# Kernel optimization log

Hardware: AMD Instinct MI355X
Metric: run time of the kernel (lower is better)

The kernel has to match this reference:

```python
import jax, jax.numpy as jnp
from jax import lax
import numpy as np

N, T, D_IN = 2048, 256, 3
H, I, D_OUT = 256, 512, 5


def setup_inputs() -> dict:
    key = jax.random.key(0)
    ks = jax.random.split(key, 9)
    s_h = 1.0 / np.sqrt(H)
    s_i = 1.0 / np.sqrt(I)
    return {
        "x": jax.random.normal(ks[0], (N, T, D_IN), dtype=jnp.float32),
        # PyTorch LSTMCell params, gate order i,f,g,o stacked along dim 0
        "W_ih": jax.random.uniform(ks[1], (4 * H, D_IN), jnp.float32, -s_h, s_h),
        "W_hh": jax.random.uniform(ks[2], (4 * H, H), jnp.float32, -s_h, s_h),
        "b_ih": jax.random.uniform(ks[3], (4 * H,), jnp.float32, -s_h, s_h),
        "b_hh": jax.random.uniform(ks[4], (4 * H,), jnp.float32, -s_h, s_h),
        "W1": jax.random.uniform(ks[5], (I, H), jnp.float32, -s_h, s_h),
        "b1": jax.random.uniform(ks[6], (I,), jnp.float32, -s_h, s_h),
        "W2": jax.random.uniform(ks[7], (D_OUT, I), jnp.float32, -s_i, s_i),
        "b2": jax.random.uniform(ks[8], (D_OUT,), jnp.float32, -s_i, s_i),
    }


def reference(x, W_ih, W_hh, b_ih, b_hh, W1, b1, W2, b2):
    n, t, _ = x.shape
    h_dim = W_hh.shape[1]
    # Precompute input contribution to gates for all timesteps: [T, N, 4H]
    xg = jnp.einsum('ntd,gd->tng', x, W_ih) + (b_ih + b_hh)

    def step(carry, xt):
        h, c = carry
        gates = xt + h @ W_hh.T  # [N, 4H]
        i, f, g, o = jnp.split(gates, 4, axis=-1)
        i = jax.nn.sigmoid(i)
        f = jax.nn.sigmoid(f)
        g = jnp.tanh(g)
        o = jax.nn.sigmoid(o)
        c = f * c + i * g
        h = o * jnp.tanh(c)
        return (h, c), h

    h0 = jnp.zeros((n, h_dim), dtype=x.dtype)
    c0 = jnp.zeros((n, h_dim), dtype=x.dtype)
    (hs_final, cs_final), hs_stack = lax.scan(step, (h0, c0), xg)  # hs_stack [T,N,H]

    out = jax.nn.relu(hs_stack @ W1.T + b1) @ W2.T + b2  # [T, N, 5]
    return jnp.transpose(out, (1, 0, 2)), hs_final, cs_final
```

## Files before the change

### kernel.cpp

```cpp
#include <hip/hip_runtime.h>


typedef __attribute__((ext_vector_type(8))) short bf16x8;
typedef __attribute__((ext_vector_type(4))) float f32x4;
typedef __attribute__((ext_vector_type(4))) int   i32x4;
typedef unsigned long long ull;

#define HST 272
#define HBS 296
#define M1S 520
#define USHB 16384
#define HSOFF 2621440
#define CSOFF 3145728
#define I8S_OFF   0
#define I8P_OFF   131072
#define TRL_OFF   262144
#define W1_OFF    278528
#define WEIGHTS_B 573440ull
#define CSTATE_F  524288
#define STATE_B   4194304ull
#define H_OFF_B   (WEIGHTS_B + STATE_B)
#define SM_PIN 0
#define SM_TRL 131072
#define SM_HBI 139264
#define SM_HBL 147968
#define SM_XS  156672
#define SM_TOTAL 162816
#define SM_AS 0
#define SM_M1 37888
#define SM_W2 104448

__device__ __forceinline__ unsigned short f2bf(float f) {
    unsigned u = __builtin_bit_cast(unsigned, f);
    u += 0x7fffu + ((u >> 16) & 1u);
    return (unsigned short)(u >> 16);
}
__device__ __forceinline__ float bf2f(unsigned short s) {
    unsigned u = ((unsigned)s) << 16;
    return __builtin_bit_cast(float, u);
}
__device__ __forceinline__ float sigm(float v)  { return 1.0f / (1.0f + __expf(-v)); }
__device__ __forceinline__ float tanh_(float v) { return 1.0f - 2.0f / (1.0f + __expf(2.0f * v)); }
__device__ __forceinline__ f32x4 MF(bf16x8 a, bf16x8 b, f32x4 c) {
    return __builtin_amdgcn_mfma_f32_16x16x32_bf16(a, b, c, 0, 0, 0);
}
__device__ __forceinline__ i32x4 MFI(i32x4 a, i32x4 b, i32x4 c) {
    return __builtin_amdgcn_mfma_i32_16x16x64_i8(a, b, c, 0, 0, 0);
}

__global__ void __launch_bounds__(1024) prep_gates_i8(
    const float* __restrict__ Whh, char* __restrict__ ws8)
{
    const int u = (int)blockIdx.x;
    const int q = u >> 2, kt = u & 3;
    const int tid = (int)threadIdx.x;
    const int wv = tid >> 6, l = tid & 63;
    size_t base = (q < 2) ? (size_t)I8P_OFF : (size_t)I8S_OFF;
    base += (size_t)(q & 1) * 65536;
    const int col = q * 256 + wv * 16 + (l & 15);
    const int kb  = kt * 64 + (l >> 4) * 16;
    union { char c[16]; i32x4 v; } p;
#pragma unroll
    for (int e = 0; e < 16; ++e) {
        float w = Whh[col * 256 + kb + e];
        int iq = (int)rintf(w * 2032.0f);
        iq = iq > 127 ? 127 : (iq < -127 ? -127 : iq);
        p.c[e] = (char)iq;
    }
    *(i32x4*)(ws8 + base + wv * 4096 + (size_t)kt * 1024 + l * 16) = p.v;
}

__global__ void __launch_bounds__(1024) prep_trailer(
    const float* __restrict__ Wih, const float* __restrict__ bih,
    const float* __restrict__ bhh, char* __restrict__ ws8)
{
    const int col = (int)threadIdx.x;
    unsigned short* t = (unsigned short*)(ws8 + TRL_OFF);
    t[col * 4 + 0] = f2bf(Wih[col * 3 + 0]);
    t[col * 4 + 1] = f2bf(Wih[col * 3 + 1]);
    t[col * 4 + 2] = f2bf(Wih[col * 3 + 2]);
    t[col * 4 + 3] = f2bf(bih[col] + bhh[col]);
}

__global__ void __launch_bounds__(1024) prep_w1(
    const float* __restrict__ W1, const float* __restrict__ b1,
    char* __restrict__ ws8)
{
    const int u = (int)blockIdx.x;
    const int kt = u >> 1, c5 = u & 1;
    const int tid = (int)threadIdx.x;
    const int wv = tid >> 6, l = tid & 63;
    const int lcol = l & 15, kgrp = l >> 4;
    const int col = wv * 32 + c5 * 16 + lcol;
    bf16x8 v;
#pragma unroll
    for (int e = 0; e < 8; ++e) {
        int k = kt * 32 + kgrp * 8 + e;
        float f = 0.f;
        if (k < 256)       f = W1[col * 256 + k];
        else if (k == 259) f = b1[col];
        v[e] = (short)f2bf(f);
    }
    *(bf16x8*)(ws8 + W1_OFF + (size_t)u * USHB + wv * 1024 + l * 16) = v;
}

__global__ void __launch_bounds__(1024)
combo(const float* __restrict__ x, const char* __restrict__ ws8,
      unsigned short* __restrict__ HhA, unsigned short* __restrict__ HhB,
      float* __restrict__ state, const float* __restrict__ W2,
      const float* __restrict__ b2, float* __restrict__ out,
      int t0, int tcl2)
{
    __shared__ __align__(16) char smem[SM_TOTAL];
    const int TC = 1 << tcl2;
    const int tid = (int)threadIdx.x;
    const int wv  = tid >> 6;
    const int l   = tid & 63;
    const int bid = (int)blockIdx.x;

    if (bid < 128) {
        if (t0 >= 256) return;
        unsigned short* Hh = ((t0 >> tcl2) & 1) ? HhB : HhA;
        const int n0   = bid * 16;
        const int r0   = (l >> 4) * 4;
        const int hcol = wv * 16 + (l & 15);
        const int arow_b = (l & 15) * HST + (l >> 4) * 16;
        const int xw = TC * 3;

        {
            const i32x4* s4 = (const i32x4*)(ws8 + I8P_OFF);
            i32x4* d4 = (i32x4*)(smem + SM_PIN);
            for (int i = tid; i < 8192; i += 1024) d4[i] = s4[i];
        }
        ((ull*)(smem + SM_TRL))[tid] = ((const ull*)(ws8 + TRL_OFF))[tid];
        for (int i = tid; i < 4352; i += 1024) ((int*)(smem + SM_HBI))[i] = 0;
        {
            float* xs = (float*)(smem + SM_XS);
            for (int i = tid; i < 16 * xw; i += 1024) {
                int r = i / xw, c = i - r * xw;
                xs[i] = x[(size_t)(n0 + r) * 768 + (size_t)t0 * 3 + c];
            }
        }
        __syncthreads();
        if (t0 > 0) {
            for (int i = tid; i < 16 * 256; i += 1024) {
                int r = i >> 8, c = i & 255;
                float h = state[(size_t)(n0 + r) * 256 + c];
                float hs = h * 127.0f, hif = rintf(hs);
                *(char*)(smem + SM_HBI + r * HST + c) = (char)(int)hif;
                *(char*)(smem + SM_HBL + r * HST + c) = (char)(int)rintf((hs - hif) * 128.0f);
            }
        }
        float cst[4] = {0.f, 0.f, 0.f, 0.f};
        const size_t obase = (size_t)(n0 + r0) * 256 + hcol;
        if (t0 > 0) {
#pragma unroll
            for (int e = 0; e < 4; ++e) cst[e] = state[CSTATE_F + obase + (size_t)e * 256];
        }
        __syncthreads();

        const char* lwI = smem + SM_PIN + wv * 4096 + l * 16;
        const char* lwF = lwI + 65536;
        const char* gpt = ws8 + I8S_OFF + wv * 4096 + l * 16;
        const char* opt = gpt + 65536;
        const char* hA0 = smem + SM_HBI + arow_b;
        const char* hL0 = smem + SM_HBL + arow_b;
        char*       wH0 = smem + SM_HBI + r0 * HST + hcol;
        const unsigned short* trl = (const unsigned short*)(smem + SM_TRL);
        const float* xs = (const float*)(smem + SM_XS);
        const size_t hq = (size_t)(n0 + r0) * TC * 256 + hcol;
        const int eo = TC * 256;
        const float invS = 1.0f / 258064.0f, inv128 = 0.0078125f;
        float hvp[4] = {0.f, 0.f, 0.f, 0.f};

#define COLLAPSE(G, HR, LR, Q)                                                \
        { ull tv = *(const ull*)(trl + ((Q) * 256 + hcol) * 4);               \
          float w0 = bf2f((unsigned short)tv);                                \
          float w1 = bf2f((unsigned short)(tv >> 16));                        \
          float w2 = bf2f((unsigned short)(tv >> 32));                        \
          float bb = bf2f((unsigned short)(tv >> 48));                        \
          _Pragma("unroll")                                                   \
          for (int e = 0; e < 4; ++e)                                         \
              G[e] = ((float)HR[e] + (float)LR[e] * inv128) * invS            \
                     + xr0[e] * w0 + xr1[e] * w1 + xr2[e] * w2 + bb; }

#pragma clang loop unroll(disable)
        for (int s = 0; s < TC; ++s) {
            const int par = s & 1;
            const int t = t0 + s;
            const char* hA = hA0 + par * 4352;
            const char* hL = hL0 + par * 4352;
            char*       wH = wH0 + (par ^ 1) * 4352;

            if (s > 0) {
                size_t b = hq + (size_t)(s - 1) * 256;
                Hh[b]          = f2bf(hvp[0]);
                Hh[b + eo]     = f2bf(hvp[1]);
                Hh[b + 2 * eo] = f2bf(hvp[2]);
                Hh[b + 3 * eo] = f2bf(hvp[3]);
            }

            i32x4 wg0 = *(const i32x4*)(gpt);
            i32x4 wo0 = *(const i32x4*)(opt);
            i32x4 wg1 = *(const i32x4*)(gpt + 1024);
            i32x4 wo1 = *(const i32x4*)(opt + 1024);

            i32x4 z = {0, 0, 0, 0};
            i32x4 hI = z, lI = z, hF = z, lF = z;
#pragma unroll
            for (int kt = 0; kt < 4; ++kt) {
                i32x4 ah = *(const i32x4*)(hA + kt * 64);
                i32x4 al = *(const i32x4*)(hL + kt * 64);
                i32x4 wi = *(const i32x4*)(lwI + kt * 1024);
                i32x4 wf = *(const i32x4*)(lwF + kt * 1024);
                hI = MFI(ah, wi, hI);  lI = MFI(al, wi, lI);
                hF = MFI(ah, wf, hF);  lF = MFI(al, wf, lF);
            }

            float xr0[4], xr1[4], xr2[4];
#pragma unroll
            for (int e = 0; e < 4; ++e) {
                const float* xp = xs + (r0 + e) * xw + s * 3;
                xr0[e] = xp[0]; xr1[e] = xp[1]; xr2[e] = xp[2];
            }

            float gI_[4], gF_[4], iv[4], fv[4];
            COLLAPSE(gI_, hI, lI, 0)
            COLLAPSE(gF_, hF, lF, 1)
#pragma unroll
            for (int e = 0; e < 4; ++e) { iv[e] = sigm(gI_[e]); fv[e] = sigm(gF_[e]); }

            i32x4 hG = z, lG = z, hO = z, lO = z;
            i32x4 wg2 = *(const i32x4*)(gpt + 2048);
            i32x4 wo2 = *(const i32x4*)(opt + 2048);
            {
                i32x4 ah = *(const i32x4*)(hA);
                i32x4 al = *(const i32x4*)(hL);
                hG = MFI(ah, wg0, hG);  lG = MFI(al, wg0, lG);
                hO = MFI(ah, wo0, hO);  lO = MFI(al, wo0, lO);
            }
            i32x4 wg3 = *(const i32x4*)(gpt + 3072);
            i32x4 wo3 = *(const i32x4*)(opt + 3072);
            {
                i32x4 ah = *(const i32x4*)(hA + 64);
                i32x4 al = *(const i32x4*)(hL + 64);
                hG = MFI(ah, wg1, hG);  lG = MFI(al, wg1, lG);
                hO = MFI(ah, wo1, hO);  lO = MFI(al, wo1, lO);
            }
            {
                i32x4 ah = *(const i32x4*)(hA + 128);
                i32x4 al = *(const i32x4*)(hL + 128);
                hG = MFI(ah, wg2, hG);  lG = MFI(al, wg2, lG);
                hO = MFI(ah, wo2, hO);  lO = MFI(al, wo2, lO);
            }
            {
                i32x4 ah = *(const i32x4*)(hA + 192);
                i32x4 al = *(const i32x4*)(hL + 192);
                hG = MFI(ah, wg3, hG);  lG = MFI(al, wg3, lG);
                hO = MFI(ah, wo3, hO);  lO = MFI(al, wo3, lO);
            }

            float gG_[4], gO_[4], gv[4], ov[4];
            COLLAPSE(gG_, hG, lG, 2)
            COLLAPSE(gO_, hO, lO, 3)
#pragma unroll
            for (int e = 0; e < 4; ++e) { gv[e] = tanh_(gG_[e]); ov[e] = sigm(gO_[e]); }

#pragma unroll
            for (int e = 0; e < 4; ++e) {
                float cv = fv[e] * cst[e] + iv[e] * gv[e];
                cst[e] = cv;
                float hv = ov[e] * tanh_(cv);
                hvp[e] = hv;
                float hs = hv * 127.0f, hif = rintf(hs);
                wH[e * HST]        = (char)(int)hif;
                wH[e * HST + 8704] = (char)(int)rintf((hs - hif) * 128.0f);
                if (t == 255) {
                    out[HSOFF + obase + (size_t)e * 256] = hv;
                    out[CSOFF + obase + (size_t)e * 256] = cv;
                } else if (s == TC - 1) {
                    state[obase + (size_t)e * 256] = hv;
                    state[CSTATE_F + obase + (size_t)e * 256] = cv;
                }
            }
            __syncthreads();
        }
        {
            size_t b = hq + (size_t)(TC - 1) * 256;
            Hh[b]          = f2bf(hvp[0]);
            Hh[b + eo]     = f2bf(hvp[1]);
            Hh[b + 2 * eo] = f2bf(hvp[2]);
            Hh[b + 3 * eo] = f2bf(hvp[3]);
        }
#undef COLLAPSE
    } else {
        if (t0 == 0) return;
        const unsigned short* Hh = (((t0 >> tcl2) & 1) ^ 1) ? HhB : HhA;
        const int t0p = t0 - TC;
        unsigned short* As  = (unsigned short*)(smem + SM_AS);
        unsigned short* m1s = (unsigned short*)(smem + SM_M1);
        unsigned short* w2s = (unsigned short*)(smem + SM_W2);
        const int lcol = l & 15, kgrp = l >> 4;
        const int laneoff_b = wv * 1024 + l * 16;
        const char* w1u = ws8 + W1_OFF;

        for (int i = tid; i < 5 * 512; i += 1024) w2s[i] = f2bf(W2[i]);

        const int ntiles = TC >> 2;
        for (int it = 0; it < ntiles; ++it) {
            const size_t tok0 = ((size_t)(bid - 128) + (size_t)it * 128) * 64;
            __syncthreads();
            for (int i = tid; i < 2048; i += 1024) {
                int tr = i >> 5, c8 = (i & 31) * 8;
                *(bf16x8*)(&As[tr * HBS + c8]) = *(const bf16x8*)(&Hh[(tok0 + tr) * 256 + c8]);
            }
            for (int i = tid; i < 64 * 40; i += 1024) {
                int tr = i / 40, c = 256 + i % 40;
                As[tr * HBS + c] = (c == 259) ? (unsigned short)0x3F80 : (unsigned short)0;
            }
            __syncthreads();

            const char* sp = w1u + laneoff_b;
            const int arow_b = ((l & 15) * HBS + kgrp * 8) * 2;
            const char* Asb = (const char*)As;
            f32x4 a0[4], a1[4];
#pragma unroll
            for (int mt = 0; mt < 4; ++mt) { a0[mt] = (f32x4){0,0,0,0}; a1[mt] = (f32x4){0,0,0,0}; }
#pragma clang loop unroll(disable)
            for (int kt = 0; kt < 9; ++kt) {
                bf16x8 b4 = *(const bf16x8*)sp;
                bf16x8 b5 = *(const bf16x8*)(sp + USHB);
                sp += 2 * USHB;
#pragma unroll
                for (int mt = 0; mt < 4; ++mt) {
                    bf16x8 av = *(const bf16x8*)(Asb + arow_b + mt * (16 * HBS * 2) + kt * 64);
                    a0[mt] = MF(av, b4, a0[mt]);
                    a1[mt] = MF(av, b5, a1[mt]);
                }
            }
            const int r0h = (l >> 4) * 4, m0c = wv * 32 + lcol, m1c = wv * 32 + 16 + lcol;
#pragma unroll
            for (int mt = 0; mt < 4; ++mt)
#pragma unroll
                for (int e = 0; e < 4; ++e) {
                    int tr = mt * 16 + r0h + e;
                    m1s[tr * M1S + m0c] = f2bf(a0[mt][e] > 0.f ? a0[mt][e] : 0.f);
                    m1s[tr * M1S + m1c] = f2bf(a1[mt][e] > 0.f ? a1[mt][e] : 0.f);
                }
            __syncthreads();

            const int grp = tid >> 3, pl = tid & 7;
            const int gn = grp / 5, gj = grp - gn * 5;
            if (tid < 640) {
                float b2r = b2[gj];
                for (int rd = 0; rd < 4; ++rd) {
                    int tr = rd * 16 + gn;
                    float acc = 0.f;
#pragma unroll
                    for (int q = 0; q < 8; ++q) {
                        bf16x8 mv  = *(const bf16x8*)(&m1s[tr * M1S] + q * 64 + pl * 8);
                        bf16x8 wvv = *(const bf16x8*)(&w2s[gj * 512] + q * 64 + pl * 8);
#pragma unroll
                        for (int e = 0; e < 8; ++e)
                            acc += bf2f((unsigned short)mv[e]) * bf2f((unsigned short)wvv[e]);
                    }
                    acc += __shfl_xor(acc, 1);
                    acc += __shfl_xor(acc, 2);
                    acc += __shfl_xor(acc, 4);
                    if (pl == 0) {
                        size_t tok = tok0 + tr;
                        int n    = (int)(tok >> tcl2);
                        int tloc = (int)(tok & (size_t)(TC - 1));
                        out[(size_t)n * 1280 + (size_t)(t0p + tloc) * 5 + gj] = acc + b2r;
                    }
                }
            }
        }
    }
}

extern "C" void kernel_launch(void* const* d_in, const int* in_sizes, int n_in,
                              void* d_out, int out_size, void* d_ws, size_t ws_size,
                              hipStream_t stream) {
    (void)in_sizes; (void)n_in; (void)out_size;
    const float* x   = (const float*)d_in[0];
    const float* Wih = (const float*)d_in[1];
    const float* Whh = (const float*)d_in[2];
    const float* bih = (const float*)d_in[3];
    const float* bhh = (const float*)d_in[4];
    const float* W1  = (const float*)d_in[5];
    const float* b1  = (const float*)d_in[6];
    const float* W2  = (const float*)d_in[7];
    const float* b2  = (const float*)d_in[8];
    char* ws8 = (char*)d_ws;
    float* o = (float*)d_out;

    prep_gates_i8<<<16, 1024, 0, stream>>>(Whh, ws8);
    prep_trailer<<<1, 1024, 0, stream>>>(Wih, bih, bhh, ws8);
    prep_w1<<<18, 1024, 0, stream>>>(W1, b1, ws8);

    int tcl2 = (ws_size >= H_OFF_B + 2ull * 2048ull * 32ull * 256ull * 2ull) ? 5 : 4;
    const int TC = 1 << tcl2;
    float* state = (float*)(ws8 + WEIGHTS_B);
    unsigned short* HhA = (unsigned short*)(ws8 + H_OFF_B);
    unsigned short* HhB = HhA + (size_t)2048 * TC * 256;

    for (int t0 = 0; t0 <= 256; t0 += TC)
        combo<<<256, 1024, 0, stream>>>(x, ws8, HhA, HhB, state, W2, b2, o, t0, tcl2);
}
```

Baseline: 1.258 ms.

## Rebalance LDS-pinned weights and restructure LSTM step with unrolled parity loop

```diff
diff --git a/kernel.cpp b/kernel.cpp
--- a/kernel.cpp
+++ b/kernel.cpp
@@ -13,7 +13,7 @@
 #define HSOFF 2621440
 #define CSOFF 3145728
 #define I8S_OFF   0
-#define I8P_OFF   131072
+#define I8P_OFF   147456
 #define TRL_OFF   262144
 #define W1_OFF    278528
 #define WEIGHTS_B 573440ull
@@ -21,14 +21,17 @@
 #define STATE_B   4194304ull
 #define H_OFF_B   (WEIGHTS_B + STATE_B)
 #define SM_PIN 0
-#define SM_TRL 131072
-#define SM_HBI 139264
-#define SM_HBL 147968
-#define SM_XS  156672
-#define SM_TOTAL 162816
+#define SM_TRL 114688
+#define SM_HBI 131072
+#define SM_HBL 139776
+#define SM_XS  148480
+#define SM_TOTAL 156672
 #define SM_AS 0
 #define SM_M1 37888
 #define SM_W2 104448
+
+#define INVH 3.8750968e-6f
+#define INVL 3.0274194e-8f
 
 __device__ __forceinline__ unsigned short f2bf(float f) {
     unsigned u = __builtin_bit_cast(unsigned, f);
@@ -55,8 +58,12 @@
     const int q = u >> 2, kt = u & 3;
     const int tid = (int)threadIdx.x;
     const int wv = tid >> 6, l = tid & 63;
-    size_t base = (q < 2) ? (size_t)I8P_OFF : (size_t)I8S_OFF;
-    base += (size_t)(q & 1) * 65536;
+    size_t dst;
+    if (q == 0)                 dst = (size_t)I8P_OFF + wv * 7168 + (2 * kt) * 1024;
+    else if (q == 1 && kt < 3)  dst = (size_t)I8P_OFF + wv * 7168 + (2 * kt + 1) * 1024;
+    else if (q == 1)            dst = (size_t)I8S_OFF + wv * 9216 + 8 * 1024;
+    else if (q == 2)            dst = (size_t)I8S_OFF + wv * 9216 + kt * 1024;
+    else                        dst = (size_t)I8S_OFF + wv * 9216 + (4 + kt) * 1024;
     const int col = q * 256 + wv * 16 + (l & 15);
     const int kb  = kt * 64 + (l >> 4) * 16;
     union { char c[16]; i32x4 v; } p;
@@ -67,7 +74,7 @@
         iq = iq > 127 ? 127 : (iq < -127 ? -127 : iq);
         p.c[e] = (char)iq;
     }
-    *(i32x4*)(ws8 + base + wv * 4096 + (size_t)kt * 1024 + l * 16) = p.v;
+    *(i32x4*)(ws8 + dst + l * 16) = p.v;
 }
 
 __global__ void __launch_bounds__(1024) prep_trailer(
@@ -75,11 +82,11 @@
     const float* __restrict__ bhh, char* __restrict__ ws8)
 {
     const int col = (int)threadIdx.x;
-    unsigned short* t = (unsigned short*)(ws8 + TRL_OFF);
-    t[col * 4 + 0] = f2bf(Wih[col * 3 + 0]);
-    t[col * 4 + 1] = f2bf(Wih[col * 3 + 1]);
-    t[col * 4 + 2] = f2bf(Wih[col * 3 + 2]);
-    t[col * 4 + 3] = f2bf(bih[col] + bhh[col]);
+    float* t = (float*)(ws8 + TRL_OFF);
+    t[col * 4 + 0] = Wih[col * 3 + 0];
+    t[col * 4 + 1] = Wih[col * 3 + 1];
+    t[col * 4 + 2] = Wih[col * 3 + 2];
+    t[col * 4 + 3] = bih[col] + bhh[col];
 }
 
 __global__ void __launch_bounds__(1024) prep_w1(
@@ -124,21 +131,24 @@
         const int n0   = bid * 16;
         const int r0   = (l >> 4) * 4;
         const int hcol = wv * 16 + (l & 15);
-        const int arow_b = (l & 15) * HST + (l >> 4) * 16;
-        const int xw = TC * 3;
 
         {
             const i32x4* s4 = (const i32x4*)(ws8 + I8P_OFF);
             i32x4* d4 = (i32x4*)(smem + SM_PIN);
-            for (int i = tid; i < 8192; i += 1024) d4[i] = s4[i];
-        }
-        ((ull*)(smem + SM_TRL))[tid] = ((const ull*)(ws8 + TRL_OFF))[tid];
-        for (int i = tid; i < 4352; i += 1024) ((int*)(smem + SM_HBI))[i] = 0;
+            for (int i = tid; i < 7168; i += 1024) d4[i] = s4[i];
+        }
+        {
+            const ull* s8 = (const ull*)(ws8 + TRL_OFF);
+            ull* d8 = (ull*)(smem + SM_TRL);
+            d8[tid] = s8[tid]; d8[tid + 1024] = s8[tid + 1024];
+        }
+        for (int i = tid; i < 4352; i += 1024)
+            ((int*)(smem + SM_HBI))[i] = 0;
         {
             float* xs = (float*)(smem + SM_XS);
-            for (int i = tid; i < 16 * xw; i += 1024) {
-                int r = i / xw, c = i - r * xw;
-                xs[i] = x[(size_t)(n0 + r) * 768 + (size_t)t0 * 3 + c];
+            for (int i = tid; i < TC * 48; i += 1024) {
+                int s = i / 48, rem = i - s * 48, r = rem / 3, d = rem - r * 3;
+                xs[(s * 16 + r) * 4 + d] = x[(size_t)(n0 + r) * 768 + (size_t)(t0 + s) * 3 + d];
             }
         }
         __syncthreads();
@@ -146,9 +156,10 @@
             for (int i = tid; i < 16 * 256; i += 1024) {
                 int r = i >> 8, c = i & 255;
                 float h = state[(size_t)(n0 + r) * 256 + c];
-                float hs = h * 127.0f, hif = rintf(hs);
-                *(char*)(smem + SM_HBI + r * HST + c) = (char)(int)hif;
-                *(char*)(smem + SM_HBL + r * HST + c) = (char)(int)rintf((hs - hif) * 128.0f);
+                int hq = (int)rintf(h * 16256.0f);
+                int hi = (hq + 64) >> 7;
+                smem[SM_HBI + r * HST + c] = (char)hi;
+                smem[SM_HBL + r * HST + c] = (char)(hq - (hi << 7));
             }
         }
         float cst[4] = {0.f, 0.f, 0.f, 0.f};
@@ -159,140 +170,120 @@
         }
         __syncthreads();
 
-        const char* lwI = smem + SM_PIN + wv * 4096 + l * 16;
-        const char* lwF = lwI + 65536;
-        const char* gpt = ws8 + I8S_OFF + wv * 4096 + l * 16;
-        const char* opt = gpt + 65536;
-        const char* hA0 = smem + SM_HBI + arow_b;
-        const char* hL0 = smem + SM_HBL + arow_b;
-        char*       wH0 = smem + SM_HBI + r0 * HST + hcol;
-        const unsigned short* trl = (const unsigned short*)(smem + SM_TRL);
-        const float* xs = (const float*)(smem + SM_XS);
-        const size_t hq = (size_t)(n0 + r0) * TC * 256 + hcol;
-        const int eo = TC * 256;
-        const float invS = 1.0f / 258064.0f, inv128 = 0.0078125f;
+        const unsigned hbiRd = SM_HBI + (unsigned)((l & 15) * HST + (l >> 4) * 16);
+        const unsigned hblRd = SM_HBL + (unsigned)((l & 15) * HST + (l >> 4) * 16);
+        const unsigned wrb   = SM_HBI + (unsigned)(r0 * HST + hcol);
+        const unsigned pinb  = SM_PIN + (unsigned)(wv * 7168 + l * 16);
+        const unsigned trlb  = SM_TRL + (unsigned)(hcol * 16);
+        const char* gof = ws8 + I8S_OFF + wv * 9216 + l * 16;
+        unsigned short* hhp = Hh + obase;
         float hvp[4] = {0.f, 0.f, 0.f, 0.f};
 
-#define COLLAPSE(G, HR, LR, Q)                                                \
-        { ull tv = *(const ull*)(trl + ((Q) * 256 + hcol) * 4);               \
-          float w0 = bf2f((unsigned short)tv);                                \
-          float w1 = bf2f((unsigned short)(tv >> 16));                        \
-          float w2 = bf2f((unsigned short)(tv >> 32));                        \
-          float bb = bf2f((unsigned short)(tv >> 48));                        \
-          _Pragma("unroll")                                                   \
-          for (int e = 0; e < 4; ++e)                                         \
-              G[e] = ((float)HR[e] + (float)LR[e] * inv128) * invS            \
-                     + xr0[e] * w0 + xr1[e] * w1 + xr2[e] * w2 + bb; }
+#define LDSI(off) (*(const i32x4*)(smem + (off)))
+#define LDGI(off) (*(const i32x4*)(gof + (off)))
+#define COLL(G, HA, LA, Q)                                                     \
+        { f32x4 tv = *(const f32x4*)(smem + trlb + (Q) * 4096);                \
+          _Pragma("unroll")                                                    \
+          for (int e = 0; e < 4; ++e) {                                        \
+              float T = tv[3] + xr[e][0]*tv[0] + xr[e][1]*tv[1] + xr[e][2]*tv[2]; \
+              G[e] = (float)HA[e]*INVH + (float)LA[e]*INVL + T; } }
+
+#define STEP(PAR)                                                              \
+        {                                                                      \
+            const int s = ss * 2 + (PAR);                                      \
+            const int t = t0 + s;                                              \
+                                        \
+            if (s > 0) {                                                       \
+                hhp[0]   = f2bf(hvp[0]); hhp[256] = f2bf(hvp[1]);              \
+                hhp[512] = f2bf(hvp[2]); hhp[768] = f2bf(hvp[3]);              \
+                hhp += 524288;                                                 \
+            }                                                                  \
+                                      \
+            i32x4 wf3 = LDGI(8192);                                            \
+            i32x4 wg  = LDGI(0);                                               \
+            i32x4 wo  = LDGI(4096);                                            \
+                                         \
+            i32x4 z = {0,0,0,0};                                               \
+            i32x4 hI = z, lI = z, hF = z, lF = z;                              \
+            _Pragma("unroll")                                                  \
+            for (int kt = 0; kt < 4; ++kt) {                                   \
+                i32x4 ah = LDSI(hbiRd + (PAR)*4352 + kt*64);                   \
+                i32x4 al = LDSI(hblRd + (PAR)*4352 + kt*64);                   \
+                i32x4 wi = LDSI(pinb + kt*2048);                               \
+                i32x4 wf = (kt < 3) ? LDSI(pinb + kt*2048 + 1024) : wf3;       \
+                hI = MFI(ah, wi, hI);  lI = MFI(al, wi, lI);                   \
+                hF = MFI(ah, wf, hF);  lF = MFI(al, wf, lF);                   \
+            }                                                                  \
+                                                         \
+            float iv[4], fv[4];                                                \
+            {                                                                  \
+                f32x4 xr[4];                                                   \
+                _Pragma("unroll")                                              \
+                for (int e = 0; e < 4; ++e)                                    \
+                    xr[e] = *(const f32x4*)(smem + SM_XS + s*256 + r0*16 + e*16); \
+                float gI_[4], gF_[4];                                          \
+                COLL(gI_, hI, lI, 0)                                           \
+                COLL(gF_, hF, lF, 1)                                           \
+                _Pragma("unroll")                                              \
+                for (int e = 0; e < 4; ++e) { iv[e] = sigm(gI_[e]); fv[e] = sigm(gF_[e]); } \
+            }                                                                  \
+                           \
+            i32x4 hG = z, lG = z, hO = z, lO = z;                              \
+            _Pragma("unroll")                                                  \
+            for (int kt = 0; kt < 4; ++kt) {                                   \
+                i32x4 ah = LDSI(hbiRd + (PAR)*4352 + kt*64);                   \
+                i32x4 al = LDSI(hblRd + (PAR)*4352 + kt*64);                   \
+                hG = MFI(ah, wg, hG);  lG = MFI(al, wg, lG);                   \
+                if (kt < 3) wg = LDGI((kt+1)*1024);                            \
+                hO = MFI(ah, wo, hO);  lO = MFI(al, wo, lO);                   \
+                if (kt < 3) wo = LDGI(4096 + (kt+1)*1024);                     \
+            }                                                                  \
+                                                         \
+            float gv[4], ov[4];                                                \
+            {                                                                  \
+                f32x4 xr[4];                                                   \
+                _Pragma("unroll")                                              \
+                for (int e = 0; e < 4; ++e)                                    \
+                    xr[e] = *(const f32x4*)(smem + SM_XS + s*256 + r0*16 + e*16); \
+                float gG_[4], gO_[4];                                          \
+                COLL(gG_, hG, lG, 2)                                           \
+                COLL(gO_, hO, lO, 3)                                           \
+                _Pragma("unroll")                                              \
+                for (int e = 0; e < 4; ++e) { gv[e] = tanh_(gG_[e]); ov[e] = sigm(gO_[e]); } \
+            }                                                                  \
+                              \
+            _Pragma("unroll")                                                  \
+            for (int e = 0; e < 4; ++e) {                                      \
+                float cv = fv[e] * cst[e] + iv[e] * gv[e];                     \
+                cst[e] = cv;                                                   \
+                float hv = ov[e] * tanh_(cv);                                  \
+                hvp[e] = hv;                                                   \
+                int hq = (int)rintf(hv * 16256.0f);                            \
+                int hi = (hq + 64) >> 7;                                       \
+                smem[wrb + (((PAR)^1)*4352 + e*HST)]        = (char)hi;        \
+                smem[wrb + (8704 + ((PAR)^1)*4352 + e*HST)] = (char)(hq - (hi << 7)); \
+                if (t == 255) {                                                \
+                    out[HSOFF + obase + (size_t)e * 256] = hv;                 \
+                    out[CSOFF + obase + (size_t)e * 256] = cv;                 \
+                } else if (s == TC - 1) {                                      \
+                    state[obase + (size_t)e * 256] = hv;                       \
+                    state[CSTATE_F + obase + (size_t)e * 256] = cv;            \
+                }                                                              \
+            }                                                                  \
+            __syncthreads();                                                   \
+        }
 
 #pragma clang loop unroll(disable)
-        for (int s = 0; s < TC; ++s) {
-            const int par = s & 1;
-            const int t = t0 + s;
-            const char* hA = hA0 + par * 4352;
-            const char* hL = hL0 + par * 4352;
-            char*       wH = wH0 + (par ^ 1) * 4352;
-
-            if (s > 0) {
-                size_t b = hq + (size_t)(s - 1) * 256;
-                Hh[b]          = f2bf(hvp[0]);
-                Hh[b + eo]     = f2bf(hvp[1]);
-                Hh[b + 2 * eo] = f2bf(hvp[2]);
-                Hh[b + 3 * eo] = f2bf(hvp[3]);
-            }
-
-            i32x4 wg0 = *(const i32x4*)(gpt);
-            i32x4 wo0 = *(const i32x4*)(opt);
-            i32x4 wg1 = *(const i32x4*)(gpt + 1024);
-            i32x4 wo1 = *(const i32x4*)(opt + 1024);
-
-            i32x4 z = {0, 0, 0, 0};
-            i32x4 hI = z, lI = z, hF = z, lF = z;
-#pragma unroll
-            for (int kt = 0; kt < 4; ++kt) {
-                i32x4 ah = *(const i32x4*)(hA + kt * 64);
-                i32x4 al = *(const i32x4*)(hL + kt * 64);
-                i32x4 wi = *(const i32x4*)(lwI + kt * 1024);
-                i32x4 wf = *(const i32x4*)(lwF + kt * 1024);
-                hI = MFI(ah, wi, hI);  lI = MFI(al, wi, lI);
-                hF = MFI(ah, wf, hF);  lF = MFI(al, wf, lF);
-            }
-
-            float xr0[4], xr1[4], xr2[4];
-#pragma unroll
-            for (int e = 0; e < 4; ++e) {
-                const float* xp = xs + (r0 + e) * xw + s * 3;
-                xr0[e] = xp[0]; xr1[e] = xp[1]; xr2[e] = xp[2];
-            }
-
-            float gI_[4], gF_[4], iv[4], fv[4];
-            COLLAPSE(gI_, hI, lI, 0)
-            COLLAPSE(gF_, hF, lF, 1)
-#pragma unroll
-            for (int e = 0; e < 4; ++e) { iv[e] = sigm(gI_[e]); fv[e] = sigm(gF_[e]); }
-
-            i32x4 hG = z, lG = z, hO = z, lO = z;
-            i32x4 wg2 = *(const i32x4*)(gpt + 2048);
-            i32x4 wo2 = *(const i32x4*)(opt + 2048);
-            {
-                i32x4 ah = *(const i32x4*)(hA);
-                i32x4 al = *(const i32x4*)(hL);
-                hG = MFI(ah, wg0, hG);  lG = MFI(al, wg0, lG);
-                hO = MFI(ah, wo0, hO);  lO = MFI(al, wo0, lO);
-            }
-            i32x4 wg3 = *(const i32x4*)(gpt + 3072);
-            i32x4 wo3 = *(const i32x4*)(opt + 3072);
-            {
-                i32x4 ah = *(const i32x4*)(hA + 64);
-                i32x4 al = *(const i32x4*)(hL + 64);
-                hG = MFI(ah, wg1, hG);  lG = MFI(al, wg1, lG);
-                hO = MFI(ah, wo1, hO);  lO = MFI(al, wo1, lO);
-            }
-            {
-                i32x4 ah = *(const i32x4*)(hA + 128);
-                i32x4 al = *(const i32x4*)(hL + 128);
-                hG = MFI(ah, wg2, hG);  lG = MFI(al, wg2, lG);
-                hO = MFI(ah, wo2, hO);  lO = MFI(al, wo2, lO);
-            }
-            {
-                i32x4 ah = *(const i32x4*)(hA + 192);
-                i32x4 al = *(const i32x4*)(hL + 192);
-                hG = MFI(ah, wg3, hG);  lG = MFI(al, wg3, lG);
-                hO = MFI(ah, wo3, hO);  lO = MFI(al, wo3, lO);
-            }
-
-            float gG_[4], gO_[4], gv[4], ov[4];
-            COLLAPSE(gG_, hG, lG, 2)
-            COLLAPSE(gO_, hO, lO, 3)
-#pragma unroll
-            for (int e = 0; e < 4; ++e) { gv[e] = tanh_(gG_[e]); ov[e] = sigm(gO_[e]); }
-
-#pragma unroll
-            for (int e = 0; e < 4; ++e) {
-                float cv = fv[e] * cst[e] + iv[e] * gv[e];
-                cst[e] = cv;
-                float hv = ov[e] * tanh_(cv);
-                hvp[e] = hv;
-                float hs = hv * 127.0f, hif = rintf(hs);
-                wH[e * HST]        = (char)(int)hif;
-                wH[e * HST + 8704] = (char)(int)rintf((hs - hif) * 128.0f);
-                if (t == 255) {
-                    out[HSOFF + obase + (size_t)e * 256] = hv;
-                    out[CSOFF + obase + (size_t)e * 256] = cv;
-                } else if (s == TC - 1) {
-                    state[obase + (size_t)e * 256] = hv;
-                    state[CSTATE_F + obase + (size_t)e * 256] = cv;
-                }
-            }
-            __syncthreads();
-        }
-        {
-            size_t b = hq + (size_t)(TC - 1) * 256;
-            Hh[b]          = f2bf(hvp[0]);
-            Hh[b + eo]     = f2bf(hvp[1]);
-            Hh[b + 2 * eo] = f2bf(hvp[2]);
-            Hh[b + 3 * eo] = f2bf(hvp[3]);
-        }
-#undef COLLAPSE
+        for (int ss = 0; ss < TC / 2; ++ss) {
+            STEP(0)
+            STEP(1)
+        }
+        hhp[0]   = f2bf(hvp[0]); hhp[256] = f2bf(hvp[1]);
+        hhp[512] = f2bf(hvp[2]); hhp[768] = f2bf(hvp[3]);
+#undef STEP
+#undef COLL
+#undef LDSI
+#undef LDGI
     } else {
         if (t0 == 0) return;
         const unsigned short* Hh = (((t0 >> tcl2) & 1) ^ 1) ? HhB : HhA;
@@ -369,8 +360,8 @@
                     acc += __shfl_xor(acc, 4);
                     if (pl == 0) {
                         size_t tok = tok0 + tr;
-                        int n    = (int)(tok >> tcl2);
-                        int tloc = (int)(tok & (size_t)(TC - 1));
+                        int n    = (int)(tok & 2047);
+                        int tloc = (int)(tok >> 11);
                         out[(size_t)n * 1280 + (size_t)(t0p + tloc) * 5 + gj] = acc + b2r;
                     }
                 }
```

Measured after the change: 1.772 ms. 40.9% more time.
